# Performance work log

Hardware: AMD Instinct MI355X
Metric: run time of the kernel (lower is better)

## Reference

```python
import jax, jax.numpy as jnp
import numpy as np

D = 512      # embed_dim
H = 8        # num_heads
DEPTH = 3    # decoder layers
V = 10000    # vocab_size
B = 64       # batch
NIMG = 144   # image grid tokens
SEQ = 17     # caption length (get_clip_mat(17,144))
FF = 4 * D


def layer_norm(x, g, b, eps=1e-5):
    m = jnp.mean(x, axis=-1, keepdims=True)
    v = jnp.mean((x - m) ** 2, axis=-1, keepdims=True)
    return (x - m) * jax.lax.rsqrt(v + eps) * g + b


def mha(xq, xkv, wq, bq, wk, bk, wv, bv, wo, bo):
    # torch MultiHeadSelfAttention with mask=None
    Bq, Nq, Dm = xq.shape
    hd = Dm // H
    q = (xq @ wq + bq).reshape(Bq, Nq, H, hd)
    k = (xkv @ wk + bk).reshape(Bq, -1, H, hd)
    v = (xkv @ wv + bv).reshape(Bq, -1, H, hd)
    attn = jnp.einsum('bqhd,bkhd->bhqk', q, k) * (hd ** -0.5)
    attn = jax.nn.softmax(attn, axis=-1)
    out = jnp.einsum('bhqk,bkhd->bqhd', attn, v).reshape(Bq, Nq, Dm)
    return out @ wo + bo


def setup_inputs() -> dict:
    key = jax.random.key(0)
    ks = iter(jax.random.split(key, 64))
    def p(*shape):
        return jax.random.normal(next(ks), shape, dtype=jnp.float32) * 0.02
    inp = {
        'encoder_out': jax.random.normal(next(ks), (B, NIMG, D), dtype=jnp.float32),
        'w': jax.random.uniform(next(ks), (SEQ, NIMG), dtype=jnp.float32) / NIMG,
        # img2text: Linear + LayerNorm
        'i2t_w': p(D, D), 'i2t_b': jnp.zeros((D,), jnp.float32),
        'i2t_ln_g': jnp.ones((D,), jnp.float32), 'i2t_ln_b': jnp.zeros((D,), jnp.float32),
        'emb': p(V, D),                                   # word_embed table
        'gen_w': p(D, V), 'gen_b': jnp.zeros((V,), jnp.float32),  # generator
        'a_w': p(2 * D, D), 'a_b': jnp.zeros((D,), jnp.float32),  # a_embed gate
        'fln_g': jnp.ones((D,), jnp.float32), 'fln_b': jnp.zeros((D,), jnp.float32),
        # stacked per-layer params [DEPTH, ...]
        'sa_wq': p(DEPTH, D, D), 'sa_bq': jnp.zeros((DEPTH, D), jnp.float32),
        'sa_wk': p(DEPTH, D, D), 'sa_bk': jnp.zeros((DEPTH, D), jnp.float32),
        'sa_wv': p(DEPTH, D, D), 'sa_bv': jnp.zeros((DEPTH, D), jnp.float32),
        'sa_wo': p(DEPTH, D, D), 'sa_bo': jnp.zeros((DEPTH, D), jnp.float32),
        'ca_wq': p(DEPTH, D, D), 'ca_bq': jnp.zeros((DEPTH, D), jnp.float32),
        'ca_wk': p(DEPTH, D, D), 'ca_bk': jnp.zeros((DEPTH, D), jnp.float32),
        'ca_wv': p(DEPTH, D, D), 'ca_bv': jnp.zeros((DEPTH, D), jnp.float32),
        'ca_wo': p(DEPTH, D, D), 'ca_bo': jnp.zeros((DEPTH, D), jnp.float32),
        'ln1_g': jnp.ones((DEPTH, D), jnp.float32), 'ln1_b': jnp.zeros((DEPTH, D), jnp.float32),
        'ln2_g': jnp.ones((DEPTH, D), jnp.float32), 'ln2_b': jnp.zeros((DEPTH, D), jnp.float32),
        'ln3_g': jnp.ones((DEPTH, D), jnp.float32), 'ln3_b': jnp.zeros((DEPTH, D), jnp.float32),
        'fc1_w': p(DEPTH, D, FF), 'fc1_b': jnp.zeros((DEPTH, FF), jnp.float32),
        'fc2_w': p(DEPTH, FF, D), 'fc2_b': jnp.zeros((DEPTH, D), jnp.float32),
    }
    return inp


def reference(encoder_out, w, i2t_w, i2t_b, i2t_ln_g, i2t_ln_b, emb, gen_w, gen_b,
              a_w, a_b, fln_g, fln_b,
              sa_wq, sa_bq, sa_wk, sa_bk, sa_wv, sa_bv, sa_wo, sa_bo,
              ca_wq, ca_bq, ca_wk, ca_bk, ca_wv, ca_bv, ca_wo, ca_bo,
              ln1_g, ln1_b, ln2_g, ln2_b, ln3_g, ln3_b,
              fc1_w, fc1_b, fc2_w, fc2_b):
    # img2text (dropout = eval no-op)
    text_emb = layer_norm(encoder_out @ i2t_w + i2t_b, i2t_ln_g, i2t_ln_b)  # [B,NIMG,D]
    # vocab-softmax word embedding gating
    word_prob = jax.nn.softmax(jnp.einsum('bnd,vd->bnv', text_emb, emb), axis=-1)
    word_emb = text_emb + jnp.einsum('bnv,vd->bnd', word_prob, emb)
    # map 144 image tokens -> 17 caption slots
    x = jnp.einsum('sn,bnd->bsd', w, word_emb)  # [B,SEQ,D]
    x_self = x
    for i in range(DEPTH):
        sc = x
        x = mha(x, x, sa_wq[i], sa_bq[i], sa_wk[i], sa_bk[i], sa_wv[i], sa_bv[i], sa_wo[i], sa_bo[i])
        x_self = x
        x = layer_norm(x + sc, ln1_g[i], ln1_b[i])
        sc = x
        x = mha(x, encoder_out, ca_wq[i], ca_bq[i], ca_wk[i], ca_bk[i], ca_wv[i], ca_bv[i], ca_wo[i], ca_bo[i])
        x = layer_norm(x + sc, ln2_g[i], ln2_b[i])
        sc = x
        x = jax.nn.relu(x @ fc1_w[i] + fc1_b[i]) @ fc2_w[i] + fc2_b[i]
        x = layer_norm(x + sc, ln3_g[i], ln3_b[i])
    # sigmoid-gated blend of last layer output and last self-attn output
    g = jax.nn.sigmoid(jnp.concatenate([x, x_self], axis=2) @ a_w + a_b)
    x = layer_norm(x * g + x_self * (1.0 - g), fln_g, fln_b)
    out = x @ gen_w + gen_b  # [B,SEQ,V]
    return out
```

## Files before the change

### kernel.cpp

```cpp
#include <hip/hip_runtime.h>

typedef unsigned short u16;
typedef __attribute__((ext_vector_type(8))) short s16x8;
typedef __attribute__((ext_vector_type(4))) float f32x4;

__device__ __forceinline__ u16 f2bf(float x) {
    union { float f; unsigned int u; } v; v.f = x;
    return (u16)((v.u + 0x7fffu + ((v.u >> 16) & 1u)) >> 16);
}
__device__ __forceinline__ float bf2f(u16 u) {
    union { unsigned int u; float f; } v; v.u = ((unsigned int)u) << 16;
    return v.f;
}

__device__ __forceinline__ void gload_lds16(const void* g, void* l) {
    __builtin_amdgcn_global_load_lds((const __attribute__((address_space(1))) void*)g,
                                     (__attribute__((address_space(3))) void*)l, 16, 0, 0);
}

template<int BM, int BN, int WM, int WN, int MODE>
__global__ __launch_bounds__(256)
void k_gemm(const u16* __restrict__ A, int lda, const u16* __restrict__ B, int ldb,
            float* __restrict__ Cf, int ldcf, u16* __restrict__ Cb, int ldcb,
            const float* __restrict__ bias, int relu, float* __restrict__ rowsum,
            int M, int N, int Ktot, int ksplit, long czstride)
{
    constexpr int MT = WM / 16, NT = WN / 16, WC = BN / WN;
    constexpr int AI = (BM * 4) / 256, BI = (BN * 4) / 256;
    __shared__ __align__(16) u16 As[BM * 32];
    __shared__ __align__(16) u16 Bs[BN * 32];
    int tid = threadIdx.x, w = tid >> 6, lane = tid & 63;
    int m0 = blockIdx.y * BM, n0 = blockIdx.x * BN;
    int wr = w / WC, wc = w % WC, lm = lane & 15, kq = lane >> 4;
    int kbeg = blockIdx.z * ksplit;
    int kend = kbeg + ksplit; if (kend > Ktot) kend = Ktot;
    if (czstride) Cf += (size_t)blockIdx.z * czstride;

    f32x4 acc[MT][NT] = {};

    for (int k0 = kbeg; k0 < kend; k0 += 32) {
        __syncthreads();
#pragma unroll
        for (int i = 0; i < AI; ++i) {
            int c = i * 256 + tid;
            const u16* g = A + (size_t)(m0 + (c >> 2)) * lda + k0 + ((c & 3) << 3);
            gload_lds16(g, As + (size_t)(i * 256 + w * 64) * 8);
        }
#pragma unroll
        for (int i = 0; i < BI; ++i) {
            int c = i * 256 + tid;
            const u16* g = B + (size_t)(n0 + (c >> 2)) * ldb + k0 + ((c & 3) << 3);
            gload_lds16(g, Bs + (size_t)(i * 256 + w * 64) * 8);
        }
        __syncthreads();
        s16x8 af[MT], bfr[NT];
#pragma unroll
        for (int mi = 0; mi < MT; ++mi)
            af[mi] = *(const s16x8*)&As[((wr * WM + mi * 16 + lm) << 5) + (kq << 3)];
#pragma unroll
        for (int ni = 0; ni < NT; ++ni)
            bfr[ni] = *(const s16x8*)&Bs[((wc * WN + ni * 16 + lm) << 5) + (kq << 3)];
#pragma unroll
        for (int mi = 0; mi < MT; ++mi)
#pragma unroll
            for (int ni = 0; ni < NT; ++ni)
                acc[mi][ni] = __builtin_amdgcn_mfma_f32_16x16x32_bf16(af[mi], bfr[ni], acc[mi][ni], 0, 0, 0);
    }

    if constexpr (MODE == 1) {
#pragma unroll
        for (int mi = 0; mi < MT; ++mi) {
            int rb = m0 + wr * WM + mi * 16 + kq * 4;
#pragma unroll
            for (int r = 0; r < 4; ++r) {
                int row = rb + r;
                float ps = 0.f;
#pragma unroll
                for (int ni = 0; ni < NT; ++ni) {
                    int col = n0 + wc * WN + ni * 16 + lm;
                    float e = 0.f;
                    if (col < N) { e = __expf(acc[mi][ni][r]); ps += e; }
                    if (row < M) Cb[(size_t)row * ldcb + col] = f2bf(e);
                }
                ps += __shfl_xor(ps, 1); ps += __shfl_xor(ps, 2);
                ps += __shfl_xor(ps, 4); ps += __shfl_xor(ps, 8);
                if (lm == 0 && row < M) atomicAdd(rowsum + row, ps);
            }
        }
    } else {
#pragma unroll
        for (int mi = 0; mi < MT; ++mi) {
            int rb = m0 + wr * WM + mi * 16 + kq * 4;
#pragma unroll
            for (int ni = 0; ni < NT; ++ni) {
                int col = n0 + wc * WN + ni * 16 + lm;
                if (col >= N) continue;
                float bv = bias ? bias[col] : 0.f;
#pragma unroll
                for (int r = 0; r < 4; ++r) {
                    int row = rb + r;
                    if (row >= M) continue;
                    float v = acc[mi][ni][r] + bv;
                    if (relu) v = fmaxf(v, 0.f);
                    if (Cf) Cf[(size_t)row * ldcf + col] = v;
                    if (Cb) Cb[(size_t)row * ldcb + col] = f2bf(v);
                }
            }
        }
    }
}

__global__ __launch_bounds__(256)
void k_transpose(const float* __restrict__ in, long in_zs, u16* __restrict__ out, long out_zs,
                 int R, int C, int Rpad, int Cpad, int ldout)
{
    __shared__ float tile[32][33];
    const float* src = in + (size_t)blockIdx.z * in_zs;
    u16* dst = out + (size_t)blockIdx.z * out_zs;
    int c0 = blockIdx.x * 32, r0 = blockIdx.y * 32;
    int tx = threadIdx.x, ty = threadIdx.y;
#pragma unroll
    for (int i = 0; i < 32; i += 8) {
        int r = r0 + ty + i, c = c0 + tx;
        tile[ty + i][tx] = (r < R && c < C) ? src[(size_t)r * C + c] : 0.f;
    }
    __syncthreads();
#pragma unroll
    for (int i = 0; i < 32; i += 8) {
        int c = c0 + ty + i, r = r0 + tx;
        if (c < Cpad && r < Rpad) dst[(size_t)c * ldout + r] = f2bf(tile[tx][ty + i]);
    }
}

__global__ __launch_bounds__(256)
void k_cvt(const float* __restrict__ in, u16* __restrict__ out, int n)
{
    for (int i = blockIdx.x * 256 + threadIdx.x; i < n; i += gridDim.x * 256)
        out[i] = f2bf(in[i]);
}

__global__ __launch_bounds__(256)
void k_zero(float* __restrict__ p, int n)
{
    int i = blockIdx.x * 256 + threadIdx.x;
    if (i < n) p[i] = 0.f;
}

__global__ __launch_bounds__(256)
void k_biaspack(const float* __restrict__ sbq, const float* __restrict__ sbk, const float* __restrict__ sbv,
                const float* __restrict__ cbk, const float* __restrict__ cbv,
                float* __restrict__ sout, float* __restrict__ cout)
{
    int i = blockIdx.x * 256 + threadIdx.x;
    if (i < 4608) {
        int l = i / 1536, j = i % 1536;
        sout[i] = j < 512 ? sbq[l * 512 + j] : j < 1024 ? sbk[l * 512 + j - 512] : sbv[l * 512 + j - 1024];
    }
    if (i < 3072) {
        int l = i / 1024, j = i % 1024;
        cout[i] = j < 512 ? cbk[l * 512 + j] : cbv[l * 512 + j - 512];
    }
}

__global__ __launch_bounds__(256)
void k_reduce_we(const float* __restrict__ part, long ps,
                 const float* __restrict__ text, const float* __restrict__ rs,
                 float* __restrict__ out, int n)
{
    int i = blockIdx.x * 256 + threadIdx.x;
    if (i >= n) return;
    float s = 0.f;
#pragma unroll
    for (int z = 0; z < 8; ++z) s += part[(size_t)z * ps + i];
    out[i] = text[i] + s * (1.f / rs[i >> 9]);
}

__global__ __launch_bounds__(256)
void k_ln(const float* __restrict__ xin, const float* __restrict__ res,
          const float* __restrict__ g, const float* __restrict__ b,
          float* __restrict__ out, u16* __restrict__ out_bf, int ldbf)
{
    int row = blockIdx.x, t = threadIdx.x;
    size_t base = (size_t)row * 512;
    float v0 = xin[base + t], v1 = xin[base + t + 256];
    if (res) { v0 += res[base + t]; v1 += res[base + t + 256]; }
    float s1 = v0 + v1, s2 = v0 * v0 + v1 * v1;
#pragma unroll
    for (int o = 32; o > 0; o >>= 1) { s1 += __shfl_down(s1, o); s2 += __shfl_down(s2, o); }
    __shared__ float a1[4], a2[4], mr[2];
    if ((t & 63) == 0) { a1[t >> 6] = s1; a2[t >> 6] = s2; }
    __syncthreads();
    if (t == 0) {
        float S1 = a1[0] + a1[1] + a1[2] + a1[3];
        float S2 = a2[0] + a2[1] + a2[2] + a2[3];
        float m = S1 * (1.f / 512.f);
        float var = S2 * (1.f / 512.f) - m * m;
        mr[0] = m; mr[1] = rsqrtf(var + 1e-5f);
    }
    __syncthreads();
    float m = mr[0], rs = mr[1];
    float y0 = (v0 - m) * rs * g[t] + b[t];
    float y1 = (v1 - m) * rs * g[t + 256] + b[t + 256];
    out[base + t] = y0; out[base + t + 256] = y1;
    if (out_bf) {
        size_t bb = (size_t)row * ldbf;
        out_bf[bb + t] = f2bf(y0); out_bf[bb + t + 256] = f2bf(y1);
    }
}

__global__ __launch_bounds__(256)
void k_wmap(const float* __restrict__ w, const float* __restrict__ we,
            float* __restrict__ x, u16* __restrict__ x_bf)
{
    int bid = blockIdx.x;
    int b = bid / 17, s = bid % 17;
    int t = threadIdx.x;
    const float* wr = w + s * 144;
    const float* base = we + (size_t)b * 144 * 512;
    float a0 = 0.f, a1 = 0.f;
    for (int n = 0; n < 144; ++n) {
        float wv = wr[n];
        a0 += wv * base[(size_t)n * 512 + t];
        a1 += wv * base[(size_t)n * 512 + t + 256];
    }
    size_t r = (size_t)(b * 17 + s);
    x[r * 512 + t] = a0; x[r * 512 + t + 256] = a1;
    x_bf[r * 1024 + t] = f2bf(a0); x_bf[r * 1024 + t + 256] = f2bf(a1);
}

__global__ __launch_bounds__(128)
void k_attn_self(const u16* __restrict__ qkv, u16* __restrict__ o)
{
    int b = blockIdx.x >> 3, h = blockIdx.x & 7;
    __shared__ float qs[17][65], ks[17][65], vs[17][65], ps[17][18];
    int t = threadIdx.x;
    for (int i = t; i < 17 * 64; i += 128) {
        int s = i >> 6, d = i & 63;
        size_t g = ((size_t)(b * 17 + s)) * 1536 + h * 64 + d;
        qs[s][d] = bf2f(qkv[g]); ks[s][d] = bf2f(qkv[g + 512]); vs[s][d] = bf2f(qkv[g + 1024]);
    }
    __syncthreads();
    for (int i = t; i < 17 * 17; i += 128) {
        int r = i / 17, c = i % 17;
        float a = 0.f;
#pragma unroll
        for (int d = 0; d < 64; ++d) a += qs[r][d] * ks[c][d];
        ps[r][c] = a * 0.125f;
    }
    __syncthreads();
    if (t < 17) {
        float mxv = -1e30f;
        for (int c = 0; c < 17; ++c) mxv = fmaxf(mxv, ps[t][c]);
        float sm = 0.f;
        for (int c = 0; c < 17; ++c) { float e = __expf(ps[t][c] - mxv); ps[t][c] = e; sm += e; }
        float inv = 1.f / sm;
        for (int c = 0; c < 17; ++c) ps[t][c] *= inv;
    }
    __syncthreads();
    for (int i = t; i < 17 * 64; i += 128) {
        int s = i >> 6, d = i & 63;
        float a = 0.f;
#pragma unroll
        for (int j = 0; j < 17; ++j) a += ps[s][j] * vs[j][d];
        o[((size_t)(b * 17 + s)) * 512 + h * 64 + d] = f2bf(a);
    }
}

__global__ __launch_bounds__(256)
void k_attn_cross(const u16* __restrict__ q, const u16* __restrict__ kv, u16* __restrict__ o)
{
    int b = blockIdx.x >> 3, h = blockIdx.x & 7;
    __shared__ float qs[17][65];
    __shared__ float ps[17][145];
    int t = threadIdx.x;
    for (int i = t; i < 17 * 64; i += 256) {
        int s = i >> 6, d = i & 63;
        qs[s][d] = bf2f(q[((size_t)(b * 17 + s)) * 512 + h * 64 + d]);
    }
    __syncthreads();
    for (int i = t; i < 17 * 144; i += 256) {
        int r = i / 144, c = i % 144;
        const u16* kr = kv + ((size_t)(b * 144 + c)) * 3072 + h * 64;
        float a = 0.f;
#pragma unroll
        for (int d = 0; d < 64; ++d) a += qs[r][d] * bf2f(kr[d]);
        ps[r][c] = a * 0.125f;
    }
    __syncthreads();
    if (t < 17) {
        float mxv = -1e30f;
        for (int c = 0; c < 144; ++c) mxv = fmaxf(mxv, ps[t][c]);
        float sm = 0.f;
        for (int c = 0; c < 144; ++c) { float e = __expf(ps[t][c] - mxv); ps[t][c] = e; sm += e; }
        float inv = 1.f / sm;
        for (int c = 0; c < 144; ++c) ps[t][c] *= inv;
    }
    __syncthreads();
    for (int i = t; i < 17 * 64; i += 256) {
        int s = i >> 6, d = i & 63;
        float a = 0.f;
        for (int j = 0; j < 144; ++j)
            a += ps[s][j] * bf2f(kv[((size_t)(b * 144 + j)) * 3072 + 512 + h * 64 + d]);
        o[((size_t)(b * 17 + s)) * 512 + h * 64 + d] = f2bf(a);
    }
}

__global__ __launch_bounds__(256)
void k_blend(const float* __restrict__ x, const float* __restrict__ xs,
             const float* __restrict__ gl, float* __restrict__ y, int n)
{
    int i = blockIdx.x * 256 + threadIdx.x;
    if (i < n) {
        float s = 1.f / (1.f + __expf(-gl[i]));
        y[i] = x[i] * s + xs[i] * (1.f - s);
    }
}

extern "C" void kernel_launch(void* const* d_in, const int* in_sizes, int n_in,
                              void* d_out, int out_size, void* d_ws, size_t ws_size,
                              hipStream_t stream)
{
    (void)in_sizes; (void)out_size;
    if (n_in < 39) return;
    const float* enc    = (const float*)d_in[0];
    const float* wmat   = (const float*)d_in[1];
    const float* i2t_w  = (const float*)d_in[2];
    const float* i2t_b  = (const float*)d_in[3];
    const float* i2t_g  = (const float*)d_in[4];
    const float* i2t_bb = (const float*)d_in[5];
    const float* emb    = (const float*)d_in[6];
    const float* gen_w  = (const float*)d_in[7];
    const float* gen_b  = (const float*)d_in[8];
    const float* a_w    = (const float*)d_in[9];
    const float* a_b    = (const float*)d_in[10];
    const float* fln_g  = (const float*)d_in[11];
    const float* fln_b  = (const float*)d_in[12];
    const float* sa_wq  = (const float*)d_in[13];
    const float* sa_bq  = (const float*)d_in[14];
    const float* sa_wk  = (const float*)d_in[15];
    const float* sa_bk  = (const float*)d_in[16];
    const float* sa_wv  = (const float*)d_in[17];
    const float* sa_bv  = (const float*)d_in[18];
    const float* sa_wo  = (const float*)d_in[19];
    const float* sa_bo  = (const float*)d_in[20];
    const float* ca_wq  = (const float*)d_in[21];
    const float* ca_bq  = (const float*)d_in[22];
    const float* ca_wk  = (const float*)d_in[23];
    const float* ca_bk  = (const float*)d_in[24];
    const float* ca_wv  = (const float*)d_in[25];
    const float* ca_bv  = (const float*)d_in[26];
    const float* ca_wo  = (const float*)d_in[27];
    const float* ca_bo  = (const float*)d_in[28];
    const float* ln1_g  = (const float*)d_in[29];
    const float* ln1_b  = (const float*)d_in[30];
    const float* ln2_g  = (const float*)d_in[31];
    const float* ln2_b  = (const float*)d_in[32];
    const float* ln3_g  = (const float*)d_in[33];
    const float* ln3_b  = (const float*)d_in[34];
    const float* fc1_w  = (const float*)d_in[35];
    const float* fc1_b  = (const float*)d_in[36];
    const float* fc2_w  = (const float*)d_in[37];
    const float* fc2_b  = (const float*)d_in[38];

    char* ws = (char*)d_ws;
    size_t off = 0;
    auto AL = [](size_t x) { return (x + 255) & ~(size_t)255; };
    auto alloc = [&](size_t bytes) { char* p = ws + off; off += AL(bytes); return p; };

    u16* i2t_wT  = (u16*)alloc((size_t)512 * 512 * 2);
    u16* sa_qkvT = (u16*)alloc((size_t)3 * 1536 * 512 * 2);
    u16* sa_woT  = (u16*)alloc((size_t)3 * 512 * 512 * 2);
    u16* ca_qT   = (u16*)alloc((size_t)3 * 512 * 512 * 2);
    u16* ca_kvT  = (u16*)alloc((size_t)3 * 1024 * 512 * 2);
    u16* ca_woT  = (u16*)alloc((size_t)3 * 512 * 512 * 2);
    u16* fc1T    = (u16*)alloc((size_t)3 * 2048 * 512 * 2);
    u16* fc2T    = (u16*)alloc((size_t)3 * 512 * 2048 * 2);
    u16* a_wT    = (u16*)alloc((size_t)512 * 1024 * 2);
    u16* gen_wT  = (u16*)alloc((size_t)10112 * 512 * 2);
    u16* embB    = (u16*)alloc((size_t)10112 * 512 * 2);
    u16* embT    = (u16*)alloc((size_t)512 * 10112 * 2);
    u16* enc_bf  = (u16*)alloc((size_t)9216 * 512 * 2);
    float* text_f   = (float*)alloc((size_t)9216 * 512 * 4);
    u16*   text_bf  = (u16*)alloc((size_t)9216 * 512 * 2);
    float* word_emb = (float*)alloc((size_t)9216 * 512 * 4);
    float* rowsum   = (float*)alloc(9216 * 4);
    float* sa_qkvB  = (float*)alloc(4608 * 4);
    float* ca_kvB   = (float*)alloc(3072 * 4);

    u16* enc_kv = (u16*)alloc((size_t)9216 * 3072 * 2);
    u16* xcat   = (u16*)alloc((size_t)1088 * 1024 * 2);
    u16* tqkv   = (u16*)alloc((size_t)1088 * 1536 * 2);
    u16* attnb  = (u16*)alloc((size_t)1088 * 512 * 2);
    u16* q_bf   = (u16*)alloc((size_t)1088 * 512 * 2);
    u16* ffn    = (u16*)alloc((size_t)1088 * 2048 * 2);
    float* x_f   = (float*)alloc((size_t)1088 * 512 * 4);
    float* xs_f  = (float*)alloc((size_t)1088 * 512 * 4);
    float* tmp_f = (float*)alloc((size_t)1088 * 512 * 4);
    float* glin  = (float*)alloc((size_t)1088 * 512 * 4);

    size_t lo = off;
    long budget = (ws_size > lo) ? (long)(ws_size - lo) : 0;
    long perrow = 10112L * 2 + 8L * 512 * 4;
    int chunk = (int)((budget / perrow) & ~(long)127);
    if (chunk > 9216) chunk = 9216;
    if (chunk < 128) chunk = 128;
    u16* logits = (u16*)(ws + lo);
    float* part = (float*)(ws + lo + AL((size_t)chunk * 10112 * 2));
    long pstride = (long)chunk * 512;

    dim3 tb(32, 8);
    auto T = [&](const float* in, long izs, u16* out, long ozs, int R, int C, int Rp, int Cp, int ldo, int nz) {
        k_transpose<<<dim3((Cp + 31) / 32, (Rp + 31) / 32, nz), tb, 0, stream>>>(in, izs, out, ozs, R, C, Rp, Cp, ldo);
    };
    T(i2t_w, 0, i2t_wT, 0, 512, 512, 512, 512, 512, 1);
    T(sa_wq, 512 * 512, sa_qkvT,             1536 * 512, 512, 512, 512, 512, 512, 3);
    T(sa_wk, 512 * 512, sa_qkvT + 512 * 512, 1536 * 512, 512, 512, 512, 512, 512, 3);
    T(sa_wv, 512 * 512, sa_qkvT + 1024 * 512,1536 * 512, 512, 512, 512, 512, 512, 3);
    T(sa_wo, 512 * 512, sa_woT, 512 * 512, 512, 512, 512, 512, 512, 3);
    T(ca_wq, 512 * 512, ca_qT,  512 * 512, 512, 512, 512, 512, 512, 3);
    T(ca_wk, 512 * 512, ca_kvT,             1024 * 512, 512, 512, 512, 512, 512, 3);
    T(ca_wv, 512 * 512, ca_kvT + 512 * 512, 1024 * 512, 512, 512, 512, 512, 512, 3);
    T(ca_wo, 512 * 512, ca_woT, 512 * 512, 512, 512, 512, 512, 512, 3);
    T(fc1_w, (long)512 * 2048, fc1T, (long)2048 * 512, 512, 2048, 512, 2048, 512, 3);
    T(fc2_w, (long)2048 * 512, fc2T, (long)512 * 2048, 2048, 512, 2048, 512, 2048, 3);
    T(a_w, 0, a_wT, 0, 1024, 512, 1024, 512, 1024, 1);
    T(gen_w, 0, gen_wT, 0, 512, 10000, 512, 10112, 512, 1);
    T(emb, 0, embT, 0, 10000, 512, 10112, 512, 10112, 1);
    k_cvt<<<2048, 256, 0, stream>>>(emb, embB, 10000 * 512);
    k_cvt<<<2048, 256, 0, stream>>>(enc, enc_bf, 9216 * 512);
    k_biaspack<<<18, 256, 0, stream>>>(sa_bq, sa_bk, sa_bv, ca_bk, ca_bv, sa_qkvB, ca_kvB);
    k_zero<<<36, 256, 0, stream>>>(rowsum, 9216);

    k_gemm<64, 64, 32, 32, 0><<<dim3(8, 144), 256, 0, stream>>>(
        enc_bf, 512, i2t_wT, 512, word_emb, 512, nullptr, 0, i2t_b, 0, nullptr,
        9216, 512, 512, 512, 0);
    k_ln<<<9216, 256, 0, stream>>>(word_emb, nullptr, i2t_g, i2t_bb, text_f, text_bf, 512);

    for (int r0 = 0; r0 < 9216; r0 += chunk) {
        int CR = (9216 - r0 < chunk) ? (9216 - r0) : chunk;
        k_gemm<128, 128, 64, 64, 1><<<dim3(79, CR / 128), 256, 0, stream>>>(
            text_bf + (size_t)r0 * 512, 512, embB, 512, nullptr, 0, logits, 10112,
            nullptr, 0, rowsum + r0, CR, 10000, 512, 512, 0);
        k_gemm<128, 128, 64, 64, 0><<<dim3(4, CR / 128, 8), 256, 0, stream>>>(
            logits, 10112, embT, 10112, part, 512, nullptr, 0, nullptr, 0, nullptr,
            CR, 512, 10112, 1280, pstride);
        k_reduce_we<<<(CR * 512 + 255) / 256, 256, 0, stream>>>(
            part, pstride, text_f + (size_t)r0 * 512, rowsum + r0,
            word_emb + (size_t)r0 * 512, CR * 512);
    }

    k_wmap<<<1088, 256, 0, stream>>>(wmat, word_emb, x_f, xcat);

    k_gemm<128, 128, 64, 64, 0><<<dim3(24, 72), 256, 0, stream>>>(
        enc_bf, 512, ca_kvT, 512, nullptr, 0, enc_kv, 3072, ca_kvB, 0, nullptr,
        9216, 3072, 512, 512, 0);

    for (int l = 0; l < 3; ++l) {
        size_t wo = (size_t)l * 512 * 512;
        k_gemm<64, 64, 32, 32, 0><<<dim3(24, 17), 256, 0, stream>>>(
            xcat, 1024, sa_qkvT + (size_t)l * 1536 * 512, 512, nullptr, 0, tqkv, 1536,
            sa_qkvB + l * 1536, 0, nullptr, 1088, 1536, 512, 512, 0);
        k_attn_self<<<512, 128, 0, stream>>>(tqkv, attnb);
        k_gemm<64, 64, 32, 32, 0><<<dim3(8, 17), 256, 0, stream>>>(
            attnb, 512, sa_woT + wo, 512, xs_f, 512, xcat + 512, 1024,
            sa_bo + l * 512, 0, nullptr, 1088, 512, 512, 512, 0);
        k_ln<<<1088, 256, 0, stream>>>(xs_f, x_f, ln1_g + l * 512, ln1_b + l * 512, x_f, xcat, 1024);
        k_gemm<64, 64, 32, 32, 0><<<dim3(8, 17), 256, 0, stream>>>(
            xcat, 1024, ca_qT + wo, 512, nullptr, 0, q_bf, 512,
            ca_bq + l * 512, 0, nullptr, 1088, 512, 512, 512, 0);
        k_attn_cross<<<512, 256, 0, stream>>>(q_bf, enc_kv + l * 1024, attnb);
        k_gemm<64, 64, 32, 32, 0><<<dim3(8, 17), 256, 0, stream>>>(
            attnb, 512, ca_woT + wo, 512, tmp_f, 512, nullptr, 0,
            ca_bo + l * 512, 0, nullptr, 1088, 512, 512, 512, 0);
        k_ln<<<1088, 256, 0, stream>>>(tmp_f, x_f, ln2_g + l * 512, ln2_b + l * 512, x_f, xcat, 1024);
        k_gemm<64, 64, 32, 32, 0><<<dim3(32, 17), 256, 0, stream>>>(
            xcat, 1024, fc1T + (size_t)l * 2048 * 512, 512, nullptr, 0, ffn, 2048,
            fc1_b + l * 2048, 1, nullptr, 1088, 2048, 512, 512, 0);
        k_gemm<64, 64, 32, 32, 0><<<dim3(8, 17), 256, 0, stream>>>(
            ffn, 2048, fc2T + (size_t)l * 512 * 2048, 2048, tmp_f, 512, nullptr, 0,
            fc2_b + l * 512, 0, nullptr, 1088, 512, 2048, 2048, 0);
        k_ln<<<1088, 256, 0, stream>>>(tmp_f, x_f, ln3_g + l * 512, ln3_b + l * 512, x_f, xcat, 1024);
    }

    k_gemm<64, 64, 32, 32, 0><<<dim3(8, 17), 256, 0, stream>>>(
        xcat, 1024, a_wT, 1024, glin, 512, nullptr, 0, a_b, 0, nullptr,
        1088, 512, 1024, 1024, 0);
    k_blend<<<2176, 256, 0, stream>>>(x_f, xs_f, glin, tmp_f, 1088 * 512);
    k_ln<<<1088, 256, 0, stream>>>(tmp_f, nullptr, fln_g, fln_b, x_f, xcat, 1024);

    k_gemm<64, 64, 32, 32, 0><<<dim3(157, 17), 256, 0, stream>>>(
        xcat, 1024, gen_wT, 512, (float*)d_out, 10000, nullptr, 0, gen_b, 0, nullptr,
        1088, 10000, 512, 512, 0);
}
```

Baseline: 1.579 ms.

## Replace LDS-staged GEMM with direct-to-register double-buffered MFMA GEMM

Replaces the shared-memory-staged GEMM with a kernel in which each wave loads its A and B fragments straight from global memory into registers. Each wave computes a 64x64 tile and prefetches the next K step into registers. This removes the LDS round trips and the block barriers, but it gives up data sharing between waves, so redundant global and L2 traffic rises. The vocab-softmax row sums are now written as per-column-block partials and summed by a new kernel instead of using atomics, which also removes the zeroing launch. Small decoder GEMMs switch to 128-thread blocks with 64x128 tiles.

```diff
diff --git a/kernel.cpp b/kernel.cpp
--- a/kernel.cpp
+++ b/kernel.cpp
@@ -13,87 +13,90 @@
     return v.f;
 }
 
-__device__ __forceinline__ void gload_lds16(const void* g, void* l) {
-    __builtin_amdgcn_global_load_lds((const __attribute__((address_space(1))) void*)g,
-                                     (__attribute__((address_space(3))) void*)l, 16, 0, 0);
-}
-
-template<int BM, int BN, int WM, int WN, int MODE>
-__global__ __launch_bounds__(256)
-void k_gemm(const u16* __restrict__ A, int lda, const u16* __restrict__ B, int ldb,
-            float* __restrict__ Cf, int ldcf, u16* __restrict__ Cb, int ldcb,
-            const float* __restrict__ bias, int relu, float* __restrict__ rowsum,
-            int M, int N, int Ktot, int ksplit, long czstride)
-{
-    constexpr int MT = WM / 16, NT = WN / 16, WC = BN / WN;
-    constexpr int AI = (BM * 4) / 256, BI = (BN * 4) / 256;
-    __shared__ __align__(16) u16 As[BM * 32];
-    __shared__ __align__(16) u16 Bs[BN * 32];
+template<int WGM, int WGN, int MODE>
+__global__ __launch_bounds__(WGM * WGN * 64)
+void k_gemmd(const u16* __restrict__ A, int lda, const u16* __restrict__ B, int ldb,
+             float* __restrict__ Cf, int ldcf, u16* __restrict__ Cb, int ldcb,
+             const float* __restrict__ bias, int relu, float* __restrict__ rspart,
+             int M, int N, int Brows, int Ktot, int ksplit, long czstride)
+{
     int tid = threadIdx.x, w = tid >> 6, lane = tid & 63;
-    int m0 = blockIdx.y * BM, n0 = blockIdx.x * BN;
-    int wr = w / WC, wc = w % WC, lm = lane & 15, kq = lane >> 4;
+    int wr = w / WGN, wc = w % WGN, lm = lane & 15, kq = lane >> 4;
+    int m0 = blockIdx.y * (WGM * 64), n0 = blockIdx.x * (WGN * 64);
     int kbeg = blockIdx.z * ksplit;
     int kend = kbeg + ksplit; if (kend > Ktot) kend = Ktot;
     if (czstride) Cf += (size_t)blockIdx.z * czstride;
 
-    f32x4 acc[MT][NT] = {};
-
-    for (int k0 = kbeg; k0 < kend; k0 += 32) {
-        __syncthreads();
-#pragma unroll
-        for (int i = 0; i < AI; ++i) {
-            int c = i * 256 + tid;
-            const u16* g = A + (size_t)(m0 + (c >> 2)) * lda + k0 + ((c & 3) << 3);
-            gload_lds16(g, As + (size_t)(i * 256 + w * 64) * 8);
+    const u16* ap[4]; const u16* bp[4];
+#pragma unroll
+    for (int mi = 0; mi < 4; ++mi) {
+        int r = m0 + wr * 64 + mi * 16 + lm; if (r > M - 1) r = M - 1;
+        ap[mi] = A + (size_t)r * lda + kbeg + kq * 8;
+    }
+#pragma unroll
+    for (int ni = 0; ni < 4; ++ni) {
+        int c = n0 + wc * 64 + ni * 16 + lm; if (c > Brows - 1) c = Brows - 1;
+        bp[ni] = B + (size_t)c * ldb + kbeg + kq * 8;
+    }
+
+    f32x4 acc[4][4] = {};
+    int iters = (kend - kbeg) >> 5;
+
+    s16x8 a0[4], b0[4];
+#pragma unroll
+    for (int i = 0; i < 4; ++i) {
+        a0[i] = *(const s16x8*)ap[i]; ap[i] += 32;
+        b0[i] = *(const s16x8*)bp[i]; bp[i] += 32;
+    }
+#pragma unroll 2
+    for (int it = 1; it < iters; ++it) {
+        s16x8 a1[4], b1[4];
+#pragma unroll
+        for (int i = 0; i < 4; ++i) {
+            a1[i] = *(const s16x8*)ap[i]; ap[i] += 32;
+            b1[i] = *(const s16x8*)bp[i]; bp[i] += 32;
         }
 #pragma unroll
-        for (int i = 0; i < BI; ++i) {
-            int c = i * 256 + tid;
-            const u16* g = B + (size_t)(n0 + (c >> 2)) * ldb + k0 + ((c & 3) << 3);
-            gload_lds16(g, Bs + (size_t)(i * 256 + w * 64) * 8);
-        }
-        __syncthreads();
-        s16x8 af[MT], bfr[NT];
-#pragma unroll
-        for (int mi = 0; mi < MT; ++mi)
-            af[mi] = *(const s16x8*)&As[((wr * WM + mi * 16 + lm) << 5) + (kq << 3)];
-#pragma unroll
-        for (int ni = 0; ni < NT; ++ni)
-            bfr[ni] = *(const s16x8*)&Bs[((wc * WN + ni * 16 + lm) << 5) + (kq << 3)];
-#pragma unroll
-        for (int mi = 0; mi < MT; ++mi)
-#pragma unroll
-            for (int ni = 0; ni < NT; ++ni)
-                acc[mi][ni] = __builtin_amdgcn_mfma_f32_16x16x32_bf16(af[mi], bfr[ni], acc[mi][ni], 0, 0, 0);
-    }
+        for (int mi = 0; mi < 4; ++mi)
+#pragma unroll
+            for (int ni = 0; ni < 4; ++ni)
+                acc[mi][ni] = __builtin_amdgcn_mfma_f32_16x16x32_bf16(a0[mi], b0[ni], acc[mi][ni], 0, 0, 0);
+#pragma unroll
+        for (int i = 0; i < 4; ++i) { a0[i] = a1[i]; b0[i] = b1[i]; }
+    }
+#pragma unroll
+    for (int mi = 0; mi < 4; ++mi)
+#pragma unroll
+        for (int ni = 0; ni < 4; ++ni)
+            acc[mi][ni] = __builtin_amdgcn_mfma_f32_16x16x32_bf16(a0[mi], b0[ni], acc[mi][ni], 0, 0, 0);
 
     if constexpr (MODE == 1) {
 #pragma unroll
-        for (int mi = 0; mi < MT; ++mi) {
-            int rb = m0 + wr * WM + mi * 16 + kq * 4;
+        for (int mi = 0; mi < 4; ++mi) {
+            int rb = m0 + wr * 64 + mi * 16 + kq * 4;
 #pragma unroll
             for (int r = 0; r < 4; ++r) {
                 int row = rb + r;
                 float ps = 0.f;
 #pragma unroll
-                for (int ni = 0; ni < NT; ++ni) {
-                    int col = n0 + wc * WN + ni * 16 + lm;
+                for (int ni = 0; ni < 4; ++ni) {
+                    int col = n0 + wc * 64 + ni * 16 + lm;
                     float e = 0.f;
                     if (col < N) { e = __expf(acc[mi][ni][r]); ps += e; }
                     if (row < M) Cb[(size_t)row * ldcb + col] = f2bf(e);
                 }
                 ps += __shfl_xor(ps, 1); ps += __shfl_xor(ps, 2);
                 ps += __shfl_xor(ps, 4); ps += __shfl_xor(ps, 8);
-                if (lm == 0 && row < M) atomicAdd(rowsum + row, ps);
+                if (lm == 0 && row < M) rspart[(size_t)blockIdx.x * M + row] = ps;
             }
         }
     } else {
 #pragma unroll
-        for (int mi = 0; mi < MT; ++mi) {
-            int rb = m0 + wr * WM + mi * 16 + kq * 4;
-#pragma unroll
-            for (int ni = 0; ni < NT; ++ni) {
-                int col = n0 + wc * WN + ni * 16 + lm;
+        for (int mi = 0; mi < 4; ++mi) {
+            int rb = m0 + wr * 64 + mi * 16 + kq * 4;
+#pragma unroll
+            for (int ni = 0; ni < 4; ++ni) {
+                int col = n0 + wc * 64 + ni * 16 + lm;
                 if (col >= N) continue;
                 float bv = bias ? bias[col] : 0.f;
 #pragma unroll
@@ -111,6 +114,17 @@
 }
 
 __global__ __launch_bounds__(256)
+void k_finrs(const float* __restrict__ rspart, int stride, int XB,
+             float* __restrict__ rs, int n)
+{
+    int i = blockIdx.x * 256 + threadIdx.x;
+    if (i >= n) return;
+    float s = 0.f;
+    for (int x = 0; x < XB; ++x) s += rspart[(size_t)x * stride + i];
+    rs[i] = s;
+}
+
+__global__ __launch_bounds__(256)
 void k_transpose(const float* __restrict__ in, long in_zs, u16* __restrict__ out, long out_zs,
                  int R, int C, int Rpad, int Cpad, int ldout)
 {
@@ -137,13 +151,6 @@
 {
     for (int i = blockIdx.x * 256 + threadIdx.x; i < n; i += gridDim.x * 256)
         out[i] = f2bf(in[i]);
-}
-
-__global__ __launch_bounds__(256)
-void k_zero(float* __restrict__ p, int n)
-{
-    int i = blockIdx.x * 256 + threadIdx.x;
-    if (i < n) p[i] = 0.f;
 }
 
 __global__ __launch_bounds__(256)
@@ -384,6 +391,7 @@
     u16*   text_bf  = (u16*)alloc((size_t)9216 * 512 * 2);
     float* word_emb = (float*)alloc((size_t)9216 * 512 * 4);
     float* rowsum   = (float*)alloc(9216 * 4);
+    float* rspart   = (float*)alloc((size_t)79 * 9216 * 4);
     float* sa_qkvB  = (float*)alloc(4608 * 4);
     float* ca_kvB   = (float*)alloc(3072 * 4);
 
@@ -429,21 +437,21 @@
     k_cvt<<<2048, 256, 0, stream>>>(emb, embB, 10000 * 512);
     k_cvt<<<2048, 256, 0, stream>>>(enc, enc_bf, 9216 * 512);
     k_biaspack<<<18, 256, 0, stream>>>(sa_bq, sa_bk, sa_bv, ca_bk, ca_bv, sa_qkvB, ca_kvB);
-    k_zero<<<36, 256, 0, stream>>>(rowsum, 9216);
-
-    k_gemm<64, 64, 32, 32, 0><<<dim3(8, 144), 256, 0, stream>>>(
+
+    k_gemmd<2, 2, 0><<<dim3(4, 72), 256, 0, stream>>>(
         enc_bf, 512, i2t_wT, 512, word_emb, 512, nullptr, 0, i2t_b, 0, nullptr,
-        9216, 512, 512, 512, 0);
+        9216, 512, 512, 512, 512, 0);
     k_ln<<<9216, 256, 0, stream>>>(word_emb, nullptr, i2t_g, i2t_bb, text_f, text_bf, 512);
 
     for (int r0 = 0; r0 < 9216; r0 += chunk) {
         int CR = (9216 - r0 < chunk) ? (9216 - r0) : chunk;
-        k_gemm<128, 128, 64, 64, 1><<<dim3(79, CR / 128), 256, 0, stream>>>(
+        k_gemmd<2, 2, 1><<<dim3(79, CR / 128), 256, 0, stream>>>(
             text_bf + (size_t)r0 * 512, 512, embB, 512, nullptr, 0, logits, 10112,
-            nullptr, 0, rowsum + r0, CR, 10000, 512, 512, 0);
-        k_gemm<128, 128, 64, 64, 0><<<dim3(4, CR / 128, 8), 256, 0, stream>>>(
+            nullptr, 0, rspart, CR, 10000, 10112, 512, 512, 0);
+        k_finrs<<<(CR + 255) / 256, 256, 0, stream>>>(rspart, CR, 79, rowsum + r0, CR);
+        k_gemmd<2, 2, 0><<<dim3(4, CR / 128, 8), 256, 0, stream>>>(
             logits, 10112, embT, 10112, part, 512, nullptr, 0, nullptr, 0, nullptr,
-            CR, 512, 10112, 1280, pstride);
+            CR, 512, 512, 10112, 1280, pstride);
         k_reduce_we<<<(CR * 512 + 255) / 256, 256, 0, stream>>>(
             part, pstride, text_f + (size_t)r0 * 512, rowsum + r0,
             word_emb + (size_t)r0 * 512, CR * 512);
@@ -451,44 +459,44 @@
 
     k_wmap<<<1088, 256, 0, stream>>>(wmat, word_emb, x_f, xcat);
 
-    k_gemm<128, 128, 64, 64, 0><<<dim3(24, 72), 256, 0, stream>>>(
+    k_gemmd<2, 2, 0><<<dim3(24, 72), 256, 0, stream>>>(
         enc_bf, 512, ca_kvT, 512, nullptr, 0, enc_kv, 3072, ca_kvB, 0, nullptr,
-        9216, 3072, 512, 512, 0);
+        9216, 3072, 3072, 512, 512, 0);
 
     for (int l = 0; l < 3; ++l) {
         size_t wo = (size_t)l * 512 * 512;
-        k_gemm<64, 64, 32, 32, 0><<<dim3(24, 17), 256, 0, stream>>>(
+        k_gemmd<1, 2, 0><<<dim3(12, 17), 128, 0, stream>>>(
             xcat, 1024, sa_qkvT + (size_t)l * 1536 * 512, 512, nullptr, 0, tqkv, 1536,
-            sa_qkvB + l * 1536, 0, nullptr, 1088, 1536, 512, 512, 0);
+            sa_qkvB + l * 1536, 0, nullptr, 1088, 1536, 1536, 512, 512, 0);
         k_attn_self<<<512, 128, 0, stream>>>(tqkv, attnb);
-        k_gemm<64, 64, 32, 32, 0><<<dim3(8, 17), 256, 0, stream>>>(
+        k_gemmd<1, 2, 0><<<dim3(4, 17), 128, 0, stream>>>(
             attnb, 512, sa_woT + wo, 512, xs_f, 512, xcat + 512, 1024,
-            sa_bo + l * 512, 0, nullptr, 1088, 512, 512, 512, 0);
+            sa_bo + l * 512, 0, nullptr, 1088, 512, 512, 512, 512, 0);
         k_ln<<<1088, 256, 0, stream>>>(xs_f, x_f, ln1_g + l * 512, ln1_b + l * 512, x_f, xcat, 1024);
-        k_gemm<64, 64, 32, 32, 0><<<dim3(8, 17), 256, 0, stream>>>(
+        k_gemmd<1, 2, 0><<<dim3(4, 17), 128, 0, stream>>>(
             xcat, 1024, ca_qT + wo, 512, nullptr, 0, q_bf, 512,
-            ca_bq + l * 512, 0, nullptr, 1088, 512, 512, 512, 0);
+            ca_bq + l * 512, 0, nullptr, 1088, 512, 512, 512, 512, 0);
         k_attn_cross<<<512, 256, 0, stream>>>(q_bf, enc_kv + l * 1024, attnb);
-        k_gemm<64, 64, 32, 32, 0><<<dim3(8, 17), 256, 0, stream>>>(
+        k_gemmd<1, 2, 0><<<dim3(4, 17), 128, 0, stream>>>(
             attnb, 512, ca_woT + wo, 512, tmp_f, 512, nullptr, 0,
-            ca_bo + l * 512, 0, nullptr, 1088, 512, 512, 512, 0);
+            ca_bo + l * 512, 0, nullptr, 1088, 512, 512, 512, 512, 0);
         k_ln<<<1088, 256, 0, stream>>>(tmp_f, x_f, ln2_g + l * 512, ln2_b + l * 512, x_f, xcat, 1024);
-        k_gemm<64, 64, 32, 32, 0><<<dim3(32, 17), 256, 0, stream>>>(
+        k_gemmd<1, 2, 0><<<dim3(16, 17), 128, 0, stream>>>(
             xcat, 1024, fc1T + (size_t)l * 2048 * 512, 512, nullptr, 0, ffn, 2048,
-            fc1_b + l * 2048, 1, nullptr, 1088, 2048, 512, 512, 0);
-        k_gemm<64, 64, 32, 32, 0><<<dim3(8, 17), 256, 0, stream>>>(
+            fc1_b + l * 2048, 1, nullptr, 1088, 2048, 2048, 512, 512, 0);
+        k_gemmd<1, 2, 0><<<dim3(4, 17), 128, 0, stream>>>(
             ffn, 2048, fc2T + (size_t)l * 512 * 2048, 2048, tmp_f, 512, nullptr, 0,
-            fc2_b + l * 512, 0, nullptr, 1088, 512, 2048, 2048, 0);
+            fc2_b + l * 512, 0, nullptr, 1088, 512, 512, 2048, 2048, 0);
         k_ln<<<1088, 256, 0, stream>>>(tmp_f, x_f, ln3_g + l * 512, ln3_b + l * 512, x_f, xcat, 1024);
     }
 
-    k_gemm<64, 64, 32, 32, 0><<<dim3(8, 17), 256, 0, stream>>>(
+    k_gemmd<1, 2, 0><<<dim3(4, 17), 128, 0, stream>>>(
         xcat, 1024, a_wT, 1024, glin, 512, nullptr, 0, a_b, 0, nullptr,
-        1088, 512, 1024, 1024, 0);
+        1088, 512, 512, 1024, 1024, 0);
     k_blend<<<2176, 256, 0, stream>>>(x_f, xs_f, glin, tmp_f, 1088 * 512);
     k_ln<<<1088, 256, 0, stream>>>(tmp_f, nullptr, fln_g, fln_b, x_f, xcat, 1024);
 
-    k_gemm<64, 64, 32, 32, 0><<<dim3(157, 17), 256, 0, stream>>>(
+    k_gemmd<1, 2, 0><<<dim3(79, 17), 128, 0, stream>>>(
         xcat, 1024, gen_wT, 512, (float*)d_out, 10000, nullptr, 0, gen_b, 0, nullptr,
-        1088, 10000, 512, 512, 0);
-}
+        1088, 10000, 10112, 512, 512, 0);
+}
```

Result: slower. 2.219 ms (+40.5%).
